# Optimization experiments

Measured on AMD Instinct MI355X. Metric: run time of the kernel, lower is better.

Reference implementation:

```python
import math
import jax, jax.numpy as jnp
import numpy as np

D_MODEL = 512
NUM_HEADS = 8
D_TRACK = 64
EPS = 1e-6


def setup_inputs() -> dict:
    key = jax.random.key(0)
    ks = jax.random.split(key, 8)
    B, C, T = 2, 4096, 16
    lecun = lambda k, shp: jax.random.normal(k, shp, jnp.float32) / jnp.sqrt(jnp.float32(shp[0]))
    return {
        "x": jax.random.normal(ks[0], (B, C, D_MODEL), jnp.float32),
        "track_embeddings": jax.random.normal(ks[1], (B, T, C, D_TRACK), jnp.float32),
        "norm_scale": jnp.ones((D_MODEL,), jnp.float32),
        "wq": lecun(ks[2], (D_MODEL, D_MODEL)), "bq": jnp.zeros((D_MODEL,), jnp.float32),
        "wk": lecun(ks[3], (D_TRACK, D_MODEL)), "bk": jnp.zeros((D_MODEL,), jnp.float32),
        "wv": lecun(ks[4], (D_TRACK, D_MODEL)), "bv": jnp.zeros((D_MODEL,), jnp.float32),
        "wo": lecun(ks[5], (D_MODEL, D_MODEL)), "bo": jnp.zeros((D_MODEL,), jnp.float32),
    }


def reference(x, track_embeddings, norm_scale, wq, bq, wk, bk, wv, bv, wo, bo):
    B, C, D = x.shape
    T = track_embeddings.shape[1]
    H = NUM_HEADS
    d_head = D // H
    residual = x
    # RMSNorm
    xn = x * jax.lax.rsqrt(jnp.mean(jnp.square(x), axis=-1, keepdims=True) + EPS) * norm_scale
    Q = (xn @ wq + bq).reshape(B, C, H, d_head)
    track_flat = track_embeddings.transpose(0, 2, 1, 3)  # (B, C, T, d_track)
    K = (track_flat @ wk + bk).reshape(B, C, T, H, d_head)
    V = (track_flat @ wv + bv).reshape(B, C, T, H, d_head)
    scale = 1.0 / math.sqrt(d_head)
    attn_logits = jnp.einsum('bchd,bcthd->bcht', Q, K) * scale
    attn_weights = jax.nn.softmax(attn_logits, axis=-1)
    attn_out = jnp.einsum('bcht,bcthd->bchd', attn_weights, V).reshape(B, C, D)
    return residual + attn_out @ wo + bo
```

## Files before the change

kernel.cpp:

```cpp
#include <hip/hip_runtime.h>
#include <math.h>


#define NTOK 8192

typedef __attribute__((ext_vector_type(8))) short short8;
typedef __attribute__((ext_vector_type(8))) unsigned short ushort8;
typedef __attribute__((ext_vector_type(4))) unsigned short ushort4v;
typedef __attribute__((ext_vector_type(4))) float f32x4;

__device__ __forceinline__ unsigned short f2bf(float f) {
    unsigned int u = __float_as_uint(f);
    unsigned int r = (u + 0x7fffu + ((u >> 16) & 1u)) >> 16;
    return (unsigned short)r;
}
__device__ __forceinline__ float bf2f(unsigned short s) {
    return __uint_as_float(((unsigned int)s) << 16);
}

__device__ __forceinline__ void gl_lds16(const void* g, void* l) {
    __builtin_amdgcn_global_load_lds(
        (const __attribute__((address_space(1))) unsigned int*)g,
        (__attribute__((address_space(3))) unsigned int*)l,
        16, 0, 0);
}


__global__ __launch_bounds__(256) void kprep(
    const float* __restrict__ x, const float* __restrict__ nscale,
    const float* __restrict__ wq, const float* __restrict__ bq,
    const float* __restrict__ wk, const float* __restrict__ wv,
    const float* __restrict__ bv, const float* __restrict__ wo,
    const float* __restrict__ bo,
    unsigned short* __restrict__ wqkT, float* __restrict__ bqk,
    unsigned short* __restrict__ wvoT, float* __restrict__ bvo,
    unsigned short* __restrict__ xnb)
{
    const int bid = blockIdx.x;
    const int t = threadIdx.x;
    if (bid < 64) {
        __shared__ float wkL[64][65];
        __shared__ float wqL[64][65];
        const int h = bid >> 3;
        const int i0 = (bid & 7) * 64;
        #pragma unroll
        for (int i = 0; i < 16; ++i) {
            const int idx = t + i * 256;
            const int d = idx >> 6, e = idx & 63;
            wkL[d][e] = wk[(size_t)d * 512 + h * 64 + e];
            wqL[d][e] = wq[(size_t)(i0 + d) * 512 + h * 64 + e];
        }
        __syncthreads();
        const int d = t & 63, ig = t >> 6;
        float acc[16];
        #pragma unroll
        for (int ii = 0; ii < 16; ++ii) acc[ii] = 0.f;
        for (int e = 0; e < 64; ++e) {
            const float kv = wkL[d][e];
            #pragma unroll
            for (int ii = 0; ii < 16; ++ii)
                acc[ii] += kv * wqL[ig * 16 + ii][e];
        }
        #pragma unroll
        for (int ii = 0; ii < 16; ++ii)
            wqkT[(size_t)(h * 64 + d) * 512 + i0 + ig * 16 + ii] = f2bf(acc[ii]);
        if (((bid & 7) == 0) && ig == 0) {
            float a = 0.f;
            #pragma unroll
            for (int e = 0; e < 64; ++e) a += bq[h * 64 + e] * wkL[d][e];
            bqk[h * 64 + d] = a;
        }
    } else if (bid < 128) {
        __shared__ float wvL[64][65];
        __shared__ float woL[64][65];
        const int b2 = bid - 64;
        const int h = b2 >> 3;
        const int j0 = (b2 & 7) * 64;
        #pragma unroll
        for (int i = 0; i < 16; ++i) {
            const int idx = t + i * 256;
            const int a = idx >> 6, b = idx & 63;
            wvL[a][b] = wv[(size_t)a * 512 + h * 64 + b];
            woL[a][b] = wo[(size_t)(h * 64 + a) * 512 + j0 + b];
        }
        __syncthreads();
        const int jloc = t & 63, dg = t >> 6;
        float acc[16];
        #pragma unroll
        for (int dd = 0; dd < 16; ++dd) acc[dd] = 0.f;
        for (int e = 0; e < 64; ++e) {
            const float b = woL[e][jloc];
            #pragma unroll
            for (int dd = 0; dd < 16; ++dd)
                acc[dd] += wvL[dg * 16 + dd][e] * b;
        }
        #pragma unroll
        for (int dd = 0; dd < 16; ++dd)
            wvoT[(size_t)(j0 + jloc) * 512 + h * 64 + dg * 16 + dd] = f2bf(acc[dd]);
    } else if (bid < 192) {
        const int b3 = bid - 128;
        const int j = b3 * 8 + (t >> 5);
        const int l = t & 31;
        float p = 0.f;
        #pragma unroll 4
        for (int e = l; e < 512; e += 32) p += bv[e] * wo[(size_t)e * 512 + j];
        #pragma unroll
        for (int m = 1; m < 32; m <<= 1) p += __shfl_xor(p, m, 64);
        if (l == 0) bvo[j] = bo[j] + p;
    } else {
        const int row = (bid - 192) * 4 + (t >> 6);
        const int lane = t & 63;
        const float* xr = x + (size_t)row * 512 + lane * 8;
        const float4 v0 = *reinterpret_cast<const float4*>(xr);
        const float4 v1 = *reinterpret_cast<const float4*>(xr + 4);
        float s = v0.x*v0.x + v0.y*v0.y + v0.z*v0.z + v0.w*v0.w
                + v1.x*v1.x + v1.y*v1.y + v1.z*v1.z + v1.w*v1.w;
        #pragma unroll
        for (int m = 1; m < 64; m <<= 1) s += __shfl_xor(s, m, 64);
        const float r = rsqrtf(s * (1.f / 512.f) + 1e-6f);
        const float4 s0 = *reinterpret_cast<const float4*>(nscale + lane * 8);
        const float4 s1 = *reinterpret_cast<const float4*>(nscale + lane * 8 + 4);
        ushort8 o;
        o[0] = f2bf(v0.x * r * s0.x); o[1] = f2bf(v0.y * r * s0.y);
        o[2] = f2bf(v0.z * r * s0.z); o[3] = f2bf(v0.w * r * s0.w);
        o[4] = f2bf(v1.x * r * s1.x); o[5] = f2bf(v1.y * r * s1.y);
        o[6] = f2bf(v1.z * r * s1.z); o[7] = f2bf(v1.w * r * s1.w);
        *reinterpret_cast<ushort8*>(xnb + (size_t)row * 512 + lane * 8) = o;
    }
}


template<int MODE>
__global__ __launch_bounds__(256) void kG(
    const unsigned short* __restrict__ A,
    const unsigned short* __restrict__ Bt,
    const float* __restrict__ bias,
    const float* __restrict__ resid,
    void* __restrict__ outp)
{
    __shared__ __align__(16) unsigned short Asm[128 * 64];
    __shared__ __align__(16) unsigned short Bsm[64 * 64];
    const int tid = threadIdx.x;
    const int mt = blockIdx.x >> 3, nt = blockIdx.x & 7;
    const int tok0 = mt * 128, n0 = nt * 64;
    const int w = tid >> 6, lane = tid & 63;
    const int wr = w >> 1, wc = w & 1;
    const int lrow = lane & 15, lk = lane >> 4;

    f32x4 acc[4][2] = {};
    for (int k0 = 0; k0 < 512; k0 += 64) {
        #pragma unroll
        for (int i = 0; i < 4; ++i) {
            const int f = tid + i * 256;
            const int row = f >> 3, c8 = f & 7;
            const int c8s = c8 ^ (row & 7);
            gl_lds16(A + (size_t)(tok0 + row) * 512 + k0 + c8s * 8,
                     (char*)Asm + f * 16);
        }
        #pragma unroll
        for (int i = 0; i < 2; ++i) {
            const int f = tid + i * 256;
            const int row = f >> 3, c8 = f & 7;
            const int c8s = c8 ^ (row & 7);
            gl_lds16(Bt + (size_t)(n0 + row) * 512 + k0 + c8s * 8,
                     (char*)Bsm + f * 16);
        }
        __syncthreads();
        #pragma unroll
        for (int kk = 0; kk < 2; ++kk) {
            short8 a[4], b[2];
            #pragma unroll
            for (int m = 0; m < 4; ++m) {
                const int r = wr * 64 + m * 16 + lrow;
                const int byte = (r * 128 + kk * 64 + lk * 16) ^ ((r & 7) << 4);
                a[m] = *reinterpret_cast<const short8*>((const char*)Asm + byte);
            }
            #pragma unroll
            for (int n = 0; n < 2; ++n) {
                const int r = wc * 32 + n * 16 + lrow;
                const int byte = (r * 128 + kk * 64 + lk * 16) ^ ((r & 7) << 4);
                b[n] = *reinterpret_cast<const short8*>((const char*)Bsm + byte);
            }
            #pragma unroll
            for (int m = 0; m < 4; ++m)
                #pragma unroll
                for (int n = 0; n < 2; ++n)
                    acc[m][n] = __builtin_amdgcn_mfma_f32_16x16x32_bf16(
                        a[m], b[n], acc[m][n], 0, 0, 0);
        }
        __syncthreads();
    }
    #pragma unroll
    for (int n = 0; n < 2; ++n) {
        const int ocol = n0 + wc * 32 + n * 16 + lrow;
        const float bs = bias[ocol];
        #pragma unroll
        for (int m = 0; m < 4; ++m) {
            #pragma unroll
            for (int r = 0; r < 4; ++r) {
                const int orow = tok0 + wr * 64 + m * 16 + lk * 4 + r;
                float v = acc[m][n][r] + bs;
                if (MODE == 0) {
                    ((unsigned short*)outp)[(size_t)orow * 512 + ocol] = f2bf(v);
                } else {
                    v += resid[(size_t)orow * 512 + ocol];
                    ((float*)outp)[(size_t)orow * 512 + ocol] = v;
                }
            }
        }
    }
}


__global__ __launch_bounds__(256) void k3_attn(
    const float* __restrict__ track, const unsigned short* __restrict__ qwb,
    unsigned short* __restrict__ wtfb)
{
    __shared__ float tf[16][68];
    __shared__ float qwl[8][68];
    __shared__ float lw[8][16];
    const int tid = threadIdx.x;
    const int token = blockIdx.x;
    const int b = token >> 12;
    const int c = token & 4095;
    {
        const int t = tid >> 4;
        const int d4 = (tid & 15) * 4;
        *reinterpret_cast<float4*>(&tf[t][d4]) =
            *reinterpret_cast<const float4*>(track + ((size_t)(b * 16 + t) * 4096 + c) * 64 + d4);
    }
    if (tid < 128) {
        const int h = tid >> 4;
        const int d4 = (tid & 15) * 4;
        const ushort4v q = *reinterpret_cast<const ushort4v*>(qwb + (size_t)token * 512 + h * 64 + d4);
        qwl[h][d4 + 0] = bf2f(q[0]);
        qwl[h][d4 + 1] = bf2f(q[1]);
        qwl[h][d4 + 2] = bf2f(q[2]);
        qwl[h][d4 + 3] = bf2f(q[3]);
    }
    __syncthreads();
    if (tid < 128) {
        const int h = tid >> 4, t = tid & 15;
        float acc = 0.f;
        #pragma unroll
        for (int d = 0; d < 64; ++d) acc += qwl[h][d] * tf[t][d];
        lw[h][t] = acc * 0.125f;
    }
    __syncthreads();
    if (tid < 8) {
        float mx = -1e30f;
        #pragma unroll
        for (int t = 0; t < 16; ++t) mx = fmaxf(mx, lw[tid][t]);
        float ev[16];
        float sum = 0.f;
        #pragma unroll
        for (int t = 0; t < 16; ++t) { ev[t] = expf(lw[tid][t] - mx); sum += ev[t]; }
        const float inv = 1.f / sum;
        #pragma unroll
        for (int t = 0; t < 16; ++t) lw[tid][t] = ev[t] * inv;
    }
    __syncthreads();
    #pragma unroll
    for (int pass = 0; pass < 2; ++pass) {
        const int j = tid + pass * 256;
        const int h = j >> 6, d = j & 63;
        float acc = 0.f;
        #pragma unroll
        for (int t = 0; t < 16; ++t) acc += lw[h][t] * tf[t][d];
        wtfb[(size_t)token * 512 + j] = f2bf(acc);
    }
}

extern "C" void kernel_launch(void* const* d_in, const int* in_sizes, int n_in,
                              void* d_out, int out_size, void* d_ws, size_t ws_size,
                              hipStream_t stream) {
    const float* x      = (const float*)d_in[0];
    const float* track  = (const float*)d_in[1];
    const float* nscale = (const float*)d_in[2];
    const float* wq     = (const float*)d_in[3];
    const float* bq     = (const float*)d_in[4];
    const float* wk     = (const float*)d_in[5];
    const float* wv     = (const float*)d_in[7];
    const float* bv     = (const float*)d_in[8];
    const float* wo     = (const float*)d_in[9];
    const float* bo     = (const float*)d_in[10];
    float* buf = (float*)d_out;

    char* ws = (char*)d_ws;
    unsigned short* xnb  = (unsigned short*)ws;
    unsigned short* qwb  = (unsigned short*)(ws + 8388608);
    unsigned short* wqkT = (unsigned short*)(ws + 16777216);
    unsigned short* wvoT = (unsigned short*)(ws + 17301504);
    float* bqk = (float*)(ws + 17825792);
    float* bvo = (float*)(ws + 17827840);

    kprep<<<192 + NTOK / 4, 256, 0, stream>>>(x, nscale, wq, bq, wk, wv, bv, wo, bo,
                                              wqkT, bqk, wvoT, bvo, xnb);
    kG<0><<<512, 256, 0, stream>>>(xnb, wqkT, bqk, nullptr, qwb);
    k3_attn<<<NTOK, 256, 0, stream>>>(track, qwb, xnb);
    kG<1><<<512, 256, 0, stream>>>(xnb, wvoT, bvo, x, buf);
}
```

Measured before the change: 58.77 us.

## Double-buffer GEMM LDS stages, remap blocks across XCDs, pack two tokens per attention block

The bf16 MFMA GEMM now double-buffers its A and B LDS tiles, issuing the async global-to-LDS loads for the next K slice while computing on the current one. Block indices are permuted so that neighbouring logical tiles, which share operand rows, land on the same XCD and can reuse its L2. The attention kernel now handles two tokens per 256-thread block and does the softmax with wave shuffles instead of a serial 8-thread pass, which removes one barrier and uses the threads that previously sat idle. The costs are doubled LDS use in the GEMM, which may lower occupancy, and correctness of the pipeline depends on the end-of-iteration barrier also waiting for the async loads to finish.

```diff
diff --git a/kernel.cpp b/kernel.cpp
--- a/kernel.cpp
+++ b/kernel.cpp
@@ -6,7 +6,6 @@
 
 typedef __attribute__((ext_vector_type(8))) short short8;
 typedef __attribute__((ext_vector_type(8))) unsigned short ushort8;
-typedef __attribute__((ext_vector_type(4))) unsigned short ushort4v;
 typedef __attribute__((ext_vector_type(4))) float f32x4;
 
 __device__ __forceinline__ unsigned short f2bf(float f) {
@@ -138,34 +137,45 @@
     const float* __restrict__ resid,
     void* __restrict__ outp)
 {
-    __shared__ __align__(16) unsigned short Asm[128 * 64];
-    __shared__ __align__(16) unsigned short Bsm[64 * 64];
+    __shared__ __align__(16) unsigned short Asm[2][128 * 64];
+    __shared__ __align__(16) unsigned short Bsm[2][64 * 64];
     const int tid = threadIdx.x;
-    const int mt = blockIdx.x >> 3, nt = blockIdx.x & 7;
+    const int hw = blockIdx.x;
+    const int logical = (hw & 7) * 64 + (hw >> 3);
+    const int mt = logical >> 3, nt = logical & 7;
     const int tok0 = mt * 128, n0 = nt * 64;
     const int w = tid >> 6, lane = tid & 63;
     const int wr = w >> 1, wc = w & 1;
     const int lrow = lane & 15, lk = lane >> 4;
 
-    f32x4 acc[4][2] = {};
-    for (int k0 = 0; k0 < 512; k0 += 64) {
+    const int srowA[4] = { (tid + 0) >> 3, (tid + 256) >> 3, (tid + 512) >> 3, (tid + 768) >> 3 };
+    const int sc8 = tid & 7;
+
+    auto STAGE = [&](int buf, int k0) {
         #pragma unroll
         for (int i = 0; i < 4; ++i) {
             const int f = tid + i * 256;
-            const int row = f >> 3, c8 = f & 7;
-            const int c8s = c8 ^ (row & 7);
+            const int row = srowA[i];
+            const int c8s = sc8 ^ (row & 7);
             gl_lds16(A + (size_t)(tok0 + row) * 512 + k0 + c8s * 8,
-                     (char*)Asm + f * 16);
+                     (char*)&Asm[buf][0] + f * 16);
         }
         #pragma unroll
         for (int i = 0; i < 2; ++i) {
             const int f = tid + i * 256;
-            const int row = f >> 3, c8 = f & 7;
-            const int c8s = c8 ^ (row & 7);
+            const int row = f >> 3;
+            const int c8s = sc8 ^ (row & 7);
             gl_lds16(Bt + (size_t)(n0 + row) * 512 + k0 + c8s * 8,
-                     (char*)Bsm + f * 16);
-        }
-        __syncthreads();
+                     (char*)&Bsm[buf][0] + f * 16);
+        }
+    };
+
+    f32x4 acc[4][2] = {};
+    STAGE(0, 0);
+    __syncthreads();
+    for (int it = 0; it < 8; ++it) {
+        const int cur = it & 1;
+        if (it < 7) STAGE(cur ^ 1, (it + 1) * 64);
         #pragma unroll
         for (int kk = 0; kk < 2; ++kk) {
             short8 a[4], b[2];
@@ -173,13 +183,13 @@
             for (int m = 0; m < 4; ++m) {
                 const int r = wr * 64 + m * 16 + lrow;
                 const int byte = (r * 128 + kk * 64 + lk * 16) ^ ((r & 7) << 4);
-                a[m] = *reinterpret_cast<const short8*>((const char*)Asm + byte);
+                a[m] = *reinterpret_cast<const short8*>((const char*)&Asm[cur][0] + byte);
             }
             #pragma unroll
             for (int n = 0; n < 2; ++n) {
                 const int r = wc * 32 + n * 16 + lrow;
                 const int byte = (r * 128 + kk * 64 + lk * 16) ^ ((r & 7) << 4);
-                b[n] = *reinterpret_cast<const short8*>((const char*)Bsm + byte);
+                b[n] = *reinterpret_cast<const short8*>((const char*)&Bsm[cur][0] + byte);
             }
             #pragma unroll
             for (int m = 0; m < 4; ++m)
@@ -216,57 +226,54 @@
     const float* __restrict__ track, const unsigned short* __restrict__ qwb,
     unsigned short* __restrict__ wtfb)
 {
-    __shared__ float tf[16][68];
-    __shared__ float qwl[8][68];
-    __shared__ float lw[8][16];
+    __shared__ float tf[2][16][68];
+    __shared__ float qwl[2][8][68];
+    __shared__ float lw[2][8][16];
     const int tid = threadIdx.x;
-    const int token = blockIdx.x;
+    const int tok = tid >> 7;
+    const int t2 = tid & 127;
+    const int token = blockIdx.x * 2 + tok;
     const int b = token >> 12;
     const int c = token & 4095;
+    #pragma unroll
+    for (int i = 0; i < 2; ++i) {
+        const int f = t2 + i * 128;
+        const int row = f >> 4, d4 = (f & 15) * 4;
+        *reinterpret_cast<float4*>(&tf[tok][row][d4]) =
+            *reinterpret_cast<const float4*>(track + ((size_t)(b * 16 + row) * 4096 + c) * 64 + d4);
+    }
+    if (t2 < 64) {
+        const ushort8 q = *reinterpret_cast<const ushort8*>(qwb + (size_t)token * 512 + t2 * 8);
+        #pragma unroll
+        for (int j = 0; j < 8; ++j) {
+            const int idx = t2 * 8 + j;
+            qwl[tok][idx >> 6][idx & 63] = bf2f(q[j]);
+        }
+    }
+    __syncthreads();
     {
-        const int t = tid >> 4;
-        const int d4 = (tid & 15) * 4;
-        *reinterpret_cast<float4*>(&tf[t][d4]) =
-            *reinterpret_cast<const float4*>(track + ((size_t)(b * 16 + t) * 4096 + c) * 64 + d4);
-    }
-    if (tid < 128) {
-        const int h = tid >> 4;
-        const int d4 = (tid & 15) * 4;
-        const ushort4v q = *reinterpret_cast<const ushort4v*>(qwb + (size_t)token * 512 + h * 64 + d4);
-        qwl[h][d4 + 0] = bf2f(q[0]);
-        qwl[h][d4 + 1] = bf2f(q[1]);
-        qwl[h][d4 + 2] = bf2f(q[2]);
-        qwl[h][d4 + 3] = bf2f(q[3]);
-    }
-    __syncthreads();
-    if (tid < 128) {
-        const int h = tid >> 4, t = tid & 15;
+        const int h = t2 >> 4, tt = t2 & 15;
         float acc = 0.f;
         #pragma unroll
-        for (int d = 0; d < 64; ++d) acc += qwl[h][d] * tf[t][d];
-        lw[h][t] = acc * 0.125f;
-    }
-    __syncthreads();
-    if (tid < 8) {
-        float mx = -1e30f;
-        #pragma unroll
-        for (int t = 0; t < 16; ++t) mx = fmaxf(mx, lw[tid][t]);
-        float ev[16];
-        float sum = 0.f;
-        #pragma unroll
-        for (int t = 0; t < 16; ++t) { ev[t] = expf(lw[tid][t] - mx); sum += ev[t]; }
-        const float inv = 1.f / sum;
-        #pragma unroll
-        for (int t = 0; t < 16; ++t) lw[tid][t] = ev[t] * inv;
+        for (int d = 0; d < 64; ++d) acc += qwl[tok][h][d] * tf[tok][tt][d];
+        float lg = acc * 0.125f;
+        float mx = lg;
+        #pragma unroll
+        for (int m = 1; m < 16; m <<= 1) mx = fmaxf(mx, __shfl_xor(mx, m, 64));
+        const float ev = __expf(lg - mx);
+        float sum = ev;
+        #pragma unroll
+        for (int m = 1; m < 16; m <<= 1) sum += __shfl_xor(sum, m, 64);
+        lw[tok][h][tt] = ev / sum;
     }
     __syncthreads();
     #pragma unroll
-    for (int pass = 0; pass < 2; ++pass) {
-        const int j = tid + pass * 256;
+    for (int i = 0; i < 4; ++i) {
+        const int j = t2 + i * 128;
         const int h = j >> 6, d = j & 63;
         float acc = 0.f;
         #pragma unroll
-        for (int t = 0; t < 16; ++t) acc += lw[h][t] * tf[t][d];
+        for (int t = 0; t < 16; ++t) acc += lw[tok][h][t] * tf[tok][t][d];
         wtfb[(size_t)token * 512 + j] = f2bf(acc);
     }
 }
@@ -297,6 +304,6 @@
     kprep<<<192 + NTOK / 4, 256, 0, stream>>>(x, nscale, wq, bq, wk, wv, bv, wo, bo,
                                               wqkT, bqk, wvoT, bvo, xnb);
     kG<0><<<512, 256, 0, stream>>>(xnb, wqkT, bqk, nullptr, qwb);
-    k3_attn<<<NTOK, 256, 0, stream>>>(track, qwb, xnb);
+    k3_attn<<<NTOK / 2, 256, 0, stream>>>(track, qwb, xnb);
     kG<1><<<512, 256, 0, stream>>>(xnb, wvoT, bvo, x, buf);
 }
```

Result: faster. 53.82 us (-8.4%).

## Fuse RMSNorm, Q projection, attention and output projection into one kernel

Applied to the files above, without the earlier changes.

Replaces the separate RMSNorm, two GEMM launches and the per-token attention kernel with a single kernel. Each 512-thread block handles 32 tokens, keeps normalized x, projected queries and attention output in LDS, and streams the weight matrices through double-buffered LDS tiles. This removes the bf16 intermediate round trips through global memory and three kernel launches. In exchange only 256 blocks run, and each re-reads both full weight matrices, which lowers parallelism and adds L2 weight traffic.

```diff
diff --git a/kernel.cpp b/kernel.cpp
--- a/kernel.cpp
+++ b/kernel.cpp
@@ -6,7 +6,6 @@
 
 typedef __attribute__((ext_vector_type(8))) short short8;
 typedef __attribute__((ext_vector_type(8))) unsigned short ushort8;
-typedef __attribute__((ext_vector_type(4))) unsigned short ushort4v;
 typedef __attribute__((ext_vector_type(4))) float f32x4;
 
 __device__ __forceinline__ unsigned short f2bf(float f) {
@@ -17,7 +16,6 @@
 __device__ __forceinline__ float bf2f(unsigned short s) {
     return __uint_as_float(((unsigned int)s) << 16);
 }
-
 __device__ __forceinline__ void gl_lds16(const void* g, void* l) {
     __builtin_amdgcn_global_load_lds(
         (const __attribute__((address_space(1))) unsigned int*)g,
@@ -27,14 +25,12 @@
 
 
 __global__ __launch_bounds__(256) void kprep(
-    const float* __restrict__ x, const float* __restrict__ nscale,
     const float* __restrict__ wq, const float* __restrict__ bq,
     const float* __restrict__ wk, const float* __restrict__ wv,
     const float* __restrict__ bv, const float* __restrict__ wo,
     const float* __restrict__ bo,
     unsigned short* __restrict__ wqkT, float* __restrict__ bqk,
-    unsigned short* __restrict__ wvoT, float* __restrict__ bvo,
-    unsigned short* __restrict__ xnb)
+    unsigned short* __restrict__ wvoT, float* __restrict__ bvo)
 {
     const int bid = blockIdx.x;
     const int t = threadIdx.x;
@@ -97,7 +93,7 @@
         #pragma unroll
         for (int dd = 0; dd < 16; ++dd)
             wvoT[(size_t)(j0 + jloc) * 512 + h * 64 + dg * 16 + dd] = f2bf(acc[dd]);
-    } else if (bid < 192) {
+    } else {
         const int b3 = bid - 128;
         const int j = b3 * 8 + (t >> 5);
         const int l = t & 31;
@@ -107,167 +103,242 @@
         #pragma unroll
         for (int m = 1; m < 32; m <<= 1) p += __shfl_xor(p, m, 64);
         if (l == 0) bvo[j] = bo[j] + p;
-    } else {
-        const int row = (bid - 192) * 4 + (t >> 6);
-        const int lane = t & 63;
-        const float* xr = x + (size_t)row * 512 + lane * 8;
-        const float4 v0 = *reinterpret_cast<const float4*>(xr);
-        const float4 v1 = *reinterpret_cast<const float4*>(xr + 4);
-        float s = v0.x*v0.x + v0.y*v0.y + v0.z*v0.z + v0.w*v0.w
-                + v1.x*v1.x + v1.y*v1.y + v1.z*v1.z + v1.w*v1.w;
-        #pragma unroll
-        for (int m = 1; m < 64; m <<= 1) s += __shfl_xor(s, m, 64);
-        const float r = rsqrtf(s * (1.f / 512.f) + 1e-6f);
-        const float4 s0 = *reinterpret_cast<const float4*>(nscale + lane * 8);
-        const float4 s1 = *reinterpret_cast<const float4*>(nscale + lane * 8 + 4);
-        ushort8 o;
-        o[0] = f2bf(v0.x * r * s0.x); o[1] = f2bf(v0.y * r * s0.y);
-        o[2] = f2bf(v0.z * r * s0.z); o[3] = f2bf(v0.w * r * s0.w);
-        o[4] = f2bf(v1.x * r * s1.x); o[5] = f2bf(v1.y * r * s1.y);
-        o[6] = f2bf(v1.z * r * s1.z); o[7] = f2bf(v1.w * r * s1.w);
-        *reinterpret_cast<ushort8*>(xnb + (size_t)row * 512 + lane * 8) = o;
-    }
-}
-
-
-template<int MODE>
-__global__ __launch_bounds__(256) void kG(
-    const unsigned short* __restrict__ A,
-    const unsigned short* __restrict__ Bt,
-    const float* __restrict__ bias,
-    const float* __restrict__ resid,
-    void* __restrict__ outp)
+    }
+}
+
+
+__global__ __launch_bounds__(512, 2) void kmega(
+    const float* __restrict__ x, const float* __restrict__ nscale,
+    const float* __restrict__ track,
+    const unsigned short* __restrict__ wqkT, const float* __restrict__ bqk,
+    const unsigned short* __restrict__ wvoT, const float* __restrict__ bvo,
+    float* __restrict__ out)
 {
-    __shared__ __align__(16) unsigned short Asm[128 * 64];
-    __shared__ __align__(16) unsigned short Bsm[64 * 64];
+    __shared__ __align__(16) unsigned short XN[32 * 512];
+    __shared__ __align__(16) unsigned short QW[32 * 512];
+    __shared__ __align__(16) unsigned short BT[2][512 * 32];
+
     const int tid = threadIdx.x;
-    const int mt = blockIdx.x >> 3, nt = blockIdx.x & 7;
-    const int tok0 = mt * 128, n0 = nt * 64;
     const int w = tid >> 6, lane = tid & 63;
-    const int wr = w >> 1, wc = w & 1;
-    const int lrow = lane & 15, lk = lane >> 4;
-
-    f32x4 acc[4][2] = {};
-    for (int k0 = 0; k0 < 512; k0 += 64) {
-        #pragma unroll
-        for (int i = 0; i < 4; ++i) {
-            const int f = tid + i * 256;
-            const int row = f >> 3, c8 = f & 7;
-            const int c8s = c8 ^ (row & 7);
-            gl_lds16(A + (size_t)(tok0 + row) * 512 + k0 + c8s * 8,
-                     (char*)Asm + f * 16);
-        }
-        #pragma unroll
-        for (int i = 0; i < 2; ++i) {
-            const int f = tid + i * 256;
-            const int row = f >> 3, c8 = f & 7;
-            const int c8s = c8 ^ (row & 7);
-            gl_lds16(Bt + (size_t)(n0 + row) * 512 + k0 + c8s * 8,
-                     (char*)Bsm + f * 16);
-        }
-        __syncthreads();
-        #pragma unroll
-        for (int kk = 0; kk < 2; ++kk) {
-            short8 a[4], b[2];
-            #pragma unroll
-            for (int m = 0; m < 4; ++m) {
-                const int r = wr * 64 + m * 16 + lrow;
-                const int byte = (r * 128 + kk * 64 + lk * 16) ^ ((r & 7) << 4);
-                a[m] = *reinterpret_cast<const short8*>((const char*)Asm + byte);
-            }
-            #pragma unroll
-            for (int n = 0; n < 2; ++n) {
-                const int r = wc * 32 + n * 16 + lrow;
-                const int byte = (r * 128 + kk * 64 + lk * 16) ^ ((r & 7) << 4);
-                b[n] = *reinterpret_cast<const short8*>((const char*)Bsm + byte);
-            }
-            #pragma unroll
-            for (int m = 0; m < 4; ++m)
-                #pragma unroll
-                for (int n = 0; n < 2; ++n)
-                    acc[m][n] = __builtin_amdgcn_mfma_f32_16x16x32_bf16(
-                        a[m], b[n], acc[m][n], 0, 0, 0);
-        }
-        __syncthreads();
-    }
+    const int lr = lane & 15, lk = lane >> 4;
+    const int tok0 = blockIdx.x * 32;
+
     #pragma unroll
-    for (int n = 0; n < 2; ++n) {
-        const int ocol = n0 + wc * 32 + n * 16 + lrow;
-        const float bs = bias[ocol];
-        #pragma unroll
-        for (int m = 0; m < 4; ++m) {
-            #pragma unroll
-            for (int r = 0; r < 4; ++r) {
-                const int orow = tok0 + wr * 64 + m * 16 + lk * 4 + r;
-                float v = acc[m][n][r] + bs;
-                if (MODE == 0) {
-                    ((unsigned short*)outp)[(size_t)orow * 512 + ocol] = f2bf(v);
-                } else {
-                    v += resid[(size_t)orow * 512 + ocol];
-                    ((float*)outp)[(size_t)orow * 512 + ocol] = v;
-                }
-            }
-        }
-    }
-}
-
-
-__global__ __launch_bounds__(256) void k3_attn(
-    const float* __restrict__ track, const unsigned short* __restrict__ qwb,
-    unsigned short* __restrict__ wtfb)
-{
-    __shared__ float tf[16][68];
-    __shared__ float qwl[8][68];
-    __shared__ float lw[8][16];
-    const int tid = threadIdx.x;
-    const int token = blockIdx.x;
-    const int b = token >> 12;
-    const int c = token & 4095;
+    for (int i = 0; i < 4; ++i) {
+        const int f = tid + i * 512;
+        const int n = f >> 2, c = f & 3;
+        gl_lds16(wqkT + (size_t)n * 512 + (c ^ (n & 3)) * 8,
+                 (char*)&BT[0][0] + f * 16);
+    }
+
     {
-        const int t = tid >> 4;
-        const int d4 = (tid & 15) * 4;
-        *reinterpret_cast<float4*>(&tf[t][d4]) =
-            *reinterpret_cast<const float4*>(track + ((size_t)(b * 16 + t) * 4096 + c) * 64 + d4);
-    }
-    if (tid < 128) {
-        const int h = tid >> 4;
-        const int d4 = (tid & 15) * 4;
-        const ushort4v q = *reinterpret_cast<const ushort4v*>(qwb + (size_t)token * 512 + h * 64 + d4);
-        qwl[h][d4 + 0] = bf2f(q[0]);
-        qwl[h][d4 + 1] = bf2f(q[1]);
-        qwl[h][d4 + 2] = bf2f(q[2]);
-        qwl[h][d4 + 3] = bf2f(q[3]);
+        const float4 ns0 = *reinterpret_cast<const float4*>(nscale + lane * 8);
+        const float4 ns1 = *reinterpret_cast<const float4*>(nscale + lane * 8 + 4);
+        #pragma unroll
+        for (int j = 0; j < 4; ++j) {
+            const int row = w * 4 + j;
+            const float* xr = x + (size_t)(tok0 + row) * 512 + lane * 8;
+            const float4 v0 = *reinterpret_cast<const float4*>(xr);
+            const float4 v1 = *reinterpret_cast<const float4*>(xr + 4);
+            float s = v0.x*v0.x + v0.y*v0.y + v0.z*v0.z + v0.w*v0.w
+                    + v1.x*v1.x + v1.y*v1.y + v1.z*v1.z + v1.w*v1.w;
+            #pragma unroll
+            for (int m = 1; m < 64; m <<= 1) s += __shfl_xor(s, m, 64);
+            const float r = rsqrtf(s * (1.f / 512.f) + 1e-6f);
+            ushort8 o;
+            o[0] = f2bf(v0.x * r * ns0.x); o[1] = f2bf(v0.y * r * ns0.y);
+            o[2] = f2bf(v0.z * r * ns0.z); o[3] = f2bf(v0.w * r * ns0.w);
+            o[4] = f2bf(v1.x * r * ns1.x); o[5] = f2bf(v1.y * r * ns1.y);
+            o[6] = f2bf(v1.z * r * ns1.z); o[7] = f2bf(v1.w * r * ns1.w);
+            *reinterpret_cast<ushort8*>((char*)XN + row * 1024 + ((lane ^ (row & 7)) << 4)) = o;
+        }
     }
     __syncthreads();
-    if (tid < 128) {
-        const int h = tid >> 4, t = tid & 15;
-        float acc = 0.f;
-        #pragma unroll
-        for (int d = 0; d < 64; ++d) acc += qwl[h][d] * tf[t][d];
-        lw[h][t] = acc * 0.125f;
+
+    {
+        f32x4 acc[2][4] = {};
+        for (int it = 0; it < 16; ++it) {
+            const int cur = it & 1;
+            if (it < 15) {
+                const int k0n = (it + 1) * 32;
+                #pragma unroll
+                for (int i = 0; i < 4; ++i) {
+                    const int f = tid + i * 512;
+                    const int n = f >> 2, c = f & 3;
+                    gl_lds16(wqkT + (size_t)n * 512 + k0n + (c ^ (n & 3)) * 8,
+                             (char*)&BT[cur ^ 1][0] + f * 16);
+                }
+            }
+            short8 a[2], b[4];
+            #pragma unroll
+            for (int m = 0; m < 2; ++m) {
+                const int row = m * 16 + lr;
+                a[m] = *reinterpret_cast<const short8*>(
+                    (const char*)XN + row * 1024 + (((it * 4 + lk) ^ (row & 7)) << 4));
+            }
+            #pragma unroll
+            for (int nf = 0; nf < 4; ++nf) {
+                const int n = w * 64 + nf * 16 + lr;
+                b[nf] = *reinterpret_cast<const short8*>(
+                    (const char*)&BT[cur][0] + n * 64 + ((lk ^ (n & 3)) << 4));
+            }
+            #pragma unroll
+            for (int m = 0; m < 2; ++m)
+                #pragma unroll
+                for (int nf = 0; nf < 4; ++nf)
+                    acc[m][nf] = __builtin_amdgcn_mfma_f32_16x16x32_bf16(
+                        a[m], b[nf], acc[m][nf], 0, 0, 0);
+            __syncthreads();
+        }
+        #pragma unroll
+        for (int nf = 0; nf < 4; ++nf) {
+            const int col = w * 64 + nf * 16 + lr;
+            const float bq_ = bqk[col];
+            #pragma unroll
+            for (int m = 0; m < 2; ++m)
+                #pragma unroll
+                for (int r = 0; r < 4; ++r) {
+                    const int row = m * 16 + lk * 4 + r;
+                    const int byte = row * 1024 + (((col >> 3) ^ (row & 7)) << 4) + ((col & 7) << 1);
+                    *reinterpret_cast<unsigned short*>((char*)QW + byte) =
+                        f2bf(acc[m][nf][r] + bq_);
+                }
+        }
     }
     __syncthreads();
-    if (tid < 8) {
-        float mx = -1e30f;
-        #pragma unroll
-        for (int t = 0; t < 16; ++t) mx = fmaxf(mx, lw[tid][t]);
-        float ev[16];
-        float sum = 0.f;
-        #pragma unroll
-        for (int t = 0; t < 16; ++t) { ev[t] = expf(lw[tid][t] - mx); sum += ev[t]; }
-        const float inv = 1.f / sum;
-        #pragma unroll
-        for (int t = 0; t < 16; ++t) lw[tid][t] = ev[t] * inv;
+
+    {
+        float* TF = (float*)&BT[0][0];
+        float* tfw = TF + w * 1056;
+        const int tt = lane >> 2, seg = lane & 3;
+        const int hA = lane >> 4, t16 = lane & 15;
+        const int h2 = lane >> 3, d0 = (lane & 7) * 8;
+        #pragma unroll
+        for (int j = 0; j < 4; ++j) {
+            const int tloc = w * 4 + j;
+            const int token = tok0 + tloc;
+            const int bb = token >> 12, cc = token & 4095;
+            const float* tr = track + ((size_t)(bb * 16 + tt) * 4096 + cc) * 64 + seg * 16;
+            #pragma unroll
+            for (int q = 0; q < 4; ++q) {
+                const float4 v = *reinterpret_cast<const float4*>(tr + q * 4);
+                float* dst = tfw + tt * 66 + seg * 16 + q * 4;
+                *reinterpret_cast<float2*>(dst)     = make_float2(v.x, v.y);
+                *reinterpret_cast<float2*>(dst + 2) = make_float2(v.z, v.w);
+            }
+            __builtin_amdgcn_wave_barrier();
+            __builtin_amdgcn_sched_barrier(0);
+            float aA = 0.f, aB = 0.f;
+            #pragma unroll
+            for (int ch = 0; ch < 8; ++ch) {
+                const short8 qa = *reinterpret_cast<const short8*>(
+                    (const char*)QW + tloc * 1024 + (((hA * 8 + ch) ^ (tloc & 7)) << 4));
+                const short8 qb = *reinterpret_cast<const short8*>(
+                    (const char*)QW + tloc * 1024 + ((((hA + 4) * 8 + ch) ^ (tloc & 7)) << 4));
+                #pragma unroll
+                for (int e = 0; e < 4; ++e) {
+                    const float2 tv = *reinterpret_cast<const float2*>(
+                        tfw + t16 * 66 + ch * 8 + e * 2);
+                    aA += bf2f((unsigned short)qa[e*2]) * tv.x + bf2f((unsigned short)qa[e*2+1]) * tv.y;
+                    aB += bf2f((unsigned short)qb[e*2]) * tv.x + bf2f((unsigned short)qb[e*2+1]) * tv.y;
+                }
+            }
+            aA *= 0.125f; aB *= 0.125f;
+            float mA = aA, mB = aB;
+            #pragma unroll
+            for (int msk = 1; msk < 16; msk <<= 1) {
+                mA = fmaxf(mA, __shfl_xor(mA, msk, 64));
+                mB = fmaxf(mB, __shfl_xor(mB, msk, 64));
+            }
+            const float eA = __expf(aA - mA), eB = __expf(aB - mB);
+            float sA = eA, sB = eB;
+            #pragma unroll
+            for (int msk = 1; msk < 16; msk <<= 1) {
+                sA += __shfl_xor(sA, msk, 64);
+                sB += __shfl_xor(sB, msk, 64);
+            }
+            const float lwA = eA / sA, lwB = eB / sB;
+            float o[8] = {};
+            #pragma unroll
+            for (int t = 0; t < 16; ++t) {
+                const int src = t + ((h2 & 3) << 4);
+                const float vA = __shfl(lwA, src, 64);
+                const float vB = __shfl(lwB, src, 64);
+                const float wgt = (h2 < 4) ? vA : vB;
+                #pragma unroll
+                for (int q = 0; q < 4; ++q) {
+                    const float2 tv = *reinterpret_cast<const float2*>(
+                        tfw + t * 66 + d0 + q * 2);
+                    o[q*2]   += wgt * tv.x;
+                    o[q*2+1] += wgt * tv.y;
+                }
+            }
+            ushort8 ov;
+            #pragma unroll
+            for (int e = 0; e < 8; ++e) ov[e] = f2bf(o[e]);
+            *reinterpret_cast<ushort8*>(
+                (char*)QW + tloc * 1024 + (((h2 * 8 + (lane & 7)) ^ (tloc & 7)) << 4)) = ov;
+            __builtin_amdgcn_wave_barrier();
+            __builtin_amdgcn_sched_barrier(0);
+        }
     }
     __syncthreads();
+
     #pragma unroll
-    for (int pass = 0; pass < 2; ++pass) {
-        const int j = tid + pass * 256;
-        const int h = j >> 6, d = j & 63;
-        float acc = 0.f;
-        #pragma unroll
-        for (int t = 0; t < 16; ++t) acc += lw[h][t] * tf[t][d];
-        wtfb[(size_t)token * 512 + j] = f2bf(acc);
+    for (int i = 0; i < 4; ++i) {
+        const int f = tid + i * 512;
+        const int n = f >> 2, c = f & 3;
+        gl_lds16(wvoT + (size_t)n * 512 + (c ^ (n & 3)) * 8,
+                 (char*)&BT[0][0] + f * 16);
+    }
+    __syncthreads();
+    {
+        f32x4 acc[2][4] = {};
+        for (int it = 0; it < 16; ++it) {
+            const int cur = it & 1;
+            if (it < 15) {
+                const int k0n = (it + 1) * 32;
+                #pragma unroll
+                for (int i = 0; i < 4; ++i) {
+                    const int f = tid + i * 512;
+                    const int n = f >> 2, c = f & 3;
+                    gl_lds16(wvoT + (size_t)n * 512 + k0n + (c ^ (n & 3)) * 8,
+                             (char*)&BT[cur ^ 1][0] + f * 16);
+                }
+            }
+            short8 a[2], b[4];
+            #pragma unroll
+            for (int m = 0; m < 2; ++m) {
+                const int row = m * 16 + lr;
+                a[m] = *reinterpret_cast<const short8*>(
+                    (const char*)QW + row * 1024 + (((it * 4 + lk) ^ (row & 7)) << 4));
+            }
+            #pragma unroll
+            for (int nf = 0; nf < 4; ++nf) {
+                const int n = w * 64 + nf * 16 + lr;
+                b[nf] = *reinterpret_cast<const short8*>(
+                    (const char*)&BT[cur][0] + n * 64 + ((lk ^ (n & 3)) << 4));
+            }
+            #pragma unroll
+            for (int m = 0; m < 2; ++m)
+                #pragma unroll
+                for (int nf = 0; nf < 4; ++nf)
+                    acc[m][nf] = __builtin_amdgcn_mfma_f32_16x16x32_bf16(
+                        a[m], b[nf], acc[m][nf], 0, 0, 0);
+            __syncthreads();
+        }
+        #pragma unroll
+        for (int nf = 0; nf < 4; ++nf) {
+            const int col = w * 64 + nf * 16 + lr;
+            const float bv_ = bvo[col];
+            #pragma unroll
+            for (int m = 0; m < 2; ++m)
+                #pragma unroll
+                for (int r = 0; r < 4; ++r) {
+                    const size_t off = (size_t)(tok0 + m * 16 + lk * 4 + r) * 512 + col;
+                    out[off] = acc[m][nf][r] + bv_ + x[off];
+                }
+        }
     }
 }
 
@@ -287,16 +358,11 @@
     float* buf = (float*)d_out;
 
     char* ws = (char*)d_ws;
-    unsigned short* xnb  = (unsigned short*)ws;
-    unsigned short* qwb  = (unsigned short*)(ws + 8388608);
-    unsigned short* wqkT = (unsigned short*)(ws + 16777216);
-    unsigned short* wvoT = (unsigned short*)(ws + 17301504);
-    float* bqk = (float*)(ws + 17825792);
-    float* bvo = (float*)(ws + 17827840);
-
-    kprep<<<192 + NTOK / 4, 256, 0, stream>>>(x, nscale, wq, bq, wk, wv, bv, wo, bo,
-                                              wqkT, bqk, wvoT, bvo, xnb);
-    kG<0><<<512, 256, 0, stream>>>(xnb, wqkT, bqk, nullptr, qwb);
-    k3_attn<<<NTOK, 256, 0, stream>>>(track, qwb, xnb);
-    kG<1><<<512, 256, 0, stream>>>(xnb, wvoT, bvo, x, buf);
-}
+    unsigned short* wqkT = (unsigned short*)ws;
+    unsigned short* wvoT = (unsigned short*)(ws + 524288);
+    float* bqk = (float*)(ws + 1048576);
+    float* bvo = (float*)(ws + 1050624);
+
+    kprep<<<192, 256, 0, stream>>>(wq, bq, wk, wv, bv, wo, bo, wqkT, bqk, wvoT, bvo);
+    kmega<<<256, 512, 0, stream>>>(x, nscale, track, wqkT, bqk, wvoT, bvo, buf);
+}
```

After: 60.60 us. 3.1% more time.
